# Performance work log

Measured on AMD Instinct MI355X. Metric: run time of the kernel, lower is better.

## Reference

```python
import jax, jax.numpy as jnp
import numpy as np

H, W = 48, 96          # fmap_size
HEADS, DH = 4, 128     # BoTNet attention defaults
EPS = 1e-5


def rel_to_abs(x):
    # x: (B, L, 2L-1) relative logits -> (B, L, L) absolute logits
    b, l, _ = x.shape
    x = jnp.pad(x, ((0, 0), (0, 0), (0, 1)))          # (B, L, 2L)
    x = x.reshape(b, l * 2 * l)
    x = jnp.pad(x, ((0, 0), (0, l - 1)))               # (B, (L+1)(2L-1))
    x = x.reshape(b, l + 1, 2 * l - 1)
    return x[:, :l, l - 1:]


def relative_logits_1d(q, rel_k):
    # q: (b, n, X, Y, d), rel_k: (2Y-1, d) -> (b, n, X, X, Y, Y)
    b, n, X, Y, d = q.shape
    logits = jnp.einsum('bnxyd,rd->bnxyr', q, rel_k)
    logits = rel_to_abs(logits.reshape(b * n * X, Y, 2 * Y - 1)).reshape(b, n, X, Y, Y)
    return jnp.broadcast_to(logits[:, :, :, None], (b, n, X, X, Y, Y))


def rel_pos_bias(q, rel_h, rel_w):
    # q: (b, n, H*W, d) already scaled -> (b, n, H*W, H*W)
    b, n, _, d = q.shape
    q2 = q.reshape(b, n, H, W, d)
    lw = relative_logits_1d(q2, rel_w)                     # (b,n,hq,hk,wq,wk)
    lw = lw.transpose(0, 1, 2, 4, 3, 5).reshape(b, n, H * W, H * W)
    qt = q2.transpose(0, 1, 3, 2, 4)                       # (b,n,W,H,d)
    lh = relative_logits_1d(qt, rel_h)                     # (b,n,wq,wk,hq,hk)
    lh = lh.transpose(0, 1, 4, 2, 5, 3).reshape(b, n, H * W, H * W)
    return lw + lh


def bn(x, g, b_, m, v):
    # inference-mode BatchNorm2d over channel dim of (B,C,H,W)
    inv = g * jax.lax.rsqrt(v + EPS)
    return (x - m[:, None, None]) * inv[:, None, None] + b_[:, None, None]


def reference(x, w_in, bn1_g, bn1_b, bn1_m, bn1_v, w_qkv, rel_h, rel_w,
              w_out, bn2_g, bn2_b, bn2_m, bn2_v, w_head, b_head):
    b = x.shape[0]
    # Self_Attn (BoTNet BottleBlock): 1x1 conv down-proj + BN + ReLU
    h1 = jax.nn.relu(bn(jnp.einsum('bcxy,oc->boxy', x, w_in), bn1_g, bn1_b, bn1_m, bn1_v))
    # qkv via 1x1 conv (no bias), chunk into q,k,v blocks along channels
    qkv = jnp.einsum('bcxy,oc->boxy', h1, w_qkv).reshape(b, 3, HEADS, DH, H * W)
    q = qkv[:, 0].transpose(0, 1, 3, 2) * (DH ** -0.5)     # (b, heads, HW, dh)
    k = qkv[:, 1].transpose(0, 1, 3, 2)
    v = qkv[:, 2].transpose(0, 1, 3, 2)
    sim = jnp.einsum('bhid,bhjd->bhij', q, k) + rel_pos_bias(q, rel_h, rel_w)
    attn = jax.nn.softmax(sim, axis=-1)
    out = jnp.einsum('bhij,bhjd->bhid', attn, v)           # (b, heads, HW, dh)
    out = out.transpose(0, 1, 3, 2).reshape(b, HEADS * DH, H, W)
    # 1x1 conv up-proj + BN, residual (dim==dim_out so shortcut=identity), ReLU
    h2 = bn(jnp.einsum('bcxy,oc->boxy', out, w_out), bn2_g, bn2_b, bn2_m, bn2_v)
    fm = jax.nn.relu(h2 + x)
    # Head's final 1x1 conv projection to out_planes
    return jnp.einsum('bcxy,oc->boxy', fm, w_head) + b_head[None, :, None, None]


def setup_inputs() -> dict:
    key = jax.random.key(0)
    ks = jax.random.split(key, 8)
    f = lambda k, s, sc: jax.random.normal(k, s, jnp.float32) * sc
    C_IN, C_MID, C_ATT, C_OUT = 256, 256, 64, 19
    return {
        'x': jax.random.normal(ks[0], (1, C_IN, H, W), jnp.float32),
        'w_in': f(ks[1], (C_ATT, C_IN), 0.05),
        'bn1_g': jnp.ones(C_ATT, jnp.float32), 'bn1_b': jnp.zeros(C_ATT, jnp.float32),
        'bn1_m': jnp.zeros(C_ATT, jnp.float32), 'bn1_v': jnp.ones(C_ATT, jnp.float32),
        'w_qkv': f(ks[2], (3 * HEADS * DH, C_ATT), 0.05),
        'rel_h': f(ks[3], (2 * H - 1, DH), 0.09),
        'rel_w': f(ks[4], (2 * W - 1, DH), 0.09),
        'w_out': f(ks[5], (C_MID, HEADS * DH), 0.02),
        'bn2_g': jnp.ones(C_MID, jnp.float32), 'bn2_b': jnp.zeros(C_MID, jnp.float32),
        'bn2_m': jnp.zeros(C_MID, jnp.float32), 'bn2_v': jnp.ones(C_MID, jnp.float32),
        'w_head': f(ks[6], (C_OUT, C_MID), 0.05),
        'b_head': jnp.zeros(C_OUT, jnp.float32),
    }
```

## Files before the change

kernel.cpp:

```cpp
#include <hip/hip_runtime.h>


typedef __attribute__((ext_vector_type(4))) float f32x4;
typedef __attribute__((ext_vector_type(8))) short s16x8;
typedef __attribute__((ext_vector_type(4))) unsigned short u16x4;

#define HW_N 4608
#define EPS 1e-5f
#define QSCALE 0.08838834764831845f

__device__ __forceinline__ unsigned short f2bf(float f) {
  unsigned u = __builtin_bit_cast(unsigned, f);
  u += 0x7fffu + ((u >> 16) & 1u);
  return (unsigned short)(u >> 16);
}
__device__ __forceinline__ float bf2f(unsigned short s) {
  return __builtin_bit_cast(float, ((unsigned)s) << 16);
}

__global__ __launch_bounds__(256) void conv1_kernel(
    const float* __restrict__ x, const float* __restrict__ w,
    const float* __restrict__ gg, const float* __restrict__ bb,
    const float* __restrict__ mm, const float* __restrict__ vv,
    float* __restrict__ h1)
{
  __shared__ __align__(16) unsigned char smA[16384];
  __shared__ __align__(16) unsigned char smB[16384];
  const int tid = (int)threadIdx.x;
  const int tx = tid & 15, ty = tid >> 4;
  const int p0 = (int)blockIdx.x * 64;
  float acc[4][4] = {};
  for (int ch = 0; ch < 4; ++ch) {
    __syncthreads();
#pragma unroll
    for (int pass = 0; pass < 4; ++pass) {
      int c4 = tid + pass * 256;
      int oc = c4 >> 4, cc4 = c4 & 15;
      f32x4 a = *(const f32x4*)(w + oc * 256 + ch * 64 + cc4 * 4);
#pragma unroll
      for (int k = 0; k < 4; ++k) {
        int cc = cc4 * 4 + k;
        *(float*)(smA + cc * 256 + ((oc * 4) ^ ((cc & 7) << 4))) = a[k];
      }
      int cc = c4 >> 4, pp4 = c4 & 15;
      f32x4 b = *(const f32x4*)(x + (ch * 64 + cc) * HW_N + p0 + pp4 * 4);
      *(f32x4*)(smB + cc * 256 + ((pp4 * 16) ^ ((cc & 7) << 4))) = b;
    }
    __syncthreads();
#pragma unroll 8
    for (int cc = 0; cc < 64; ++cc) {
      f32x4 av = *(const f32x4*)(smA + cc * 256 + ((ty * 16) ^ ((cc & 7) << 4)));
      f32x4 bv = *(const f32x4*)(smB + cc * 256 + ((tx * 16) ^ ((cc & 7) << 4)));
#pragma unroll
      for (int i = 0; i < 4; ++i)
#pragma unroll
        for (int j = 0; j < 4; ++j) acc[i][j] = fmaf(av[i], bv[j], acc[i][j]);
    }
  }
#pragma unroll
  for (int i = 0; i < 4; ++i) {
    int oc = ty * 4 + i;
    float inv = gg[oc] * rsqrtf(vv[oc] + EPS);
    float bia = bb[oc] - mm[oc] * inv;
    f32x4 o;
#pragma unroll
    for (int j = 0; j < 4; ++j) o[j] = fmaxf(acc[i][j] * inv + bia, 0.f);
    *(f32x4*)(h1 + oc * HW_N + p0 + tx * 4) = o;
  }
}

__global__ __launch_bounds__(256) void convqkv_kernel(
    const float* __restrict__ h1, const float* __restrict__ w,
    unsigned short* __restrict__ qb, unsigned short* __restrict__ kb,
    unsigned short* __restrict__ vb)
{
  __shared__ __align__(16) unsigned char smA[16384];
  __shared__ __align__(16) unsigned char smB[16384];
  const int tid = (int)threadIdx.x;
  const int tx = tid & 15, ty = tid >> 4;
  const int p0 = (int)blockIdx.x * 64;
  const int o0 = (int)blockIdx.y * 64;
  float acc[4][4] = {};
#pragma unroll
  for (int pass = 0; pass < 4; ++pass) {
    int c4 = tid + pass * 256;
    int oc = c4 >> 4, cc4 = c4 & 15;
    f32x4 a = *(const f32x4*)(w + (o0 + oc) * 64 + cc4 * 4);
#pragma unroll
    for (int k = 0; k < 4; ++k) {
      int cc = cc4 * 4 + k;
      *(float*)(smA + cc * 256 + ((oc * 4) ^ ((cc & 7) << 4))) = a[k];
    }
    int cc = c4 >> 4, pp4 = c4 & 15;
    f32x4 b = *(const f32x4*)(h1 + cc * HW_N + p0 + pp4 * 4);
    *(f32x4*)(smB + cc * 256 + ((pp4 * 16) ^ ((cc & 7) << 4))) = b;
  }
  __syncthreads();
#pragma unroll 8
  for (int cc = 0; cc < 64; ++cc) {
    f32x4 av = *(const f32x4*)(smA + cc * 256 + ((tx * 16) ^ ((cc & 7) << 4)));
    f32x4 bv = *(const f32x4*)(smB + cc * 256 + ((ty * 16) ^ ((cc & 7) << 4)));
#pragma unroll
    for (int i = 0; i < 4; ++i)
#pragma unroll
      for (int j = 0; j < 4; ++j) acc[i][j] = fmaf(av[i], bv[j], acc[i][j]);
  }
  const int chunk = o0 >> 9, head = (o0 >> 7) & 3, dbase = o0 & 127;
  if (chunk == 0) {
#pragma unroll
    for (int j = 0; j < 4; ++j) {
      unsigned short pk[4];
#pragma unroll
      for (int i = 0; i < 4; ++i) pk[i] = f2bf(acc[i][j] * QSCALE);
      *(unsigned long long*)(qb + (head * HW_N + p0 + ty * 4 + j) * 128 + dbase + tx * 4) =
          *(unsigned long long*)pk;
    }
  } else if (chunk == 1) {
#pragma unroll
    for (int j = 0; j < 4; ++j) {
      unsigned short pk[4];
#pragma unroll
      for (int i = 0; i < 4; ++i) pk[i] = f2bf(acc[i][j]);
      *(unsigned long long*)(kb + (head * HW_N + p0 + ty * 4 + j) * 128 + dbase + tx * 4) =
          *(unsigned long long*)pk;
    }
  } else {
#pragma unroll
    for (int i = 0; i < 4; ++i) {
      unsigned short pk[4];
#pragma unroll
      for (int j = 0; j < 4; ++j) pk[j] = f2bf(acc[i][j]);
      *(unsigned long long*)(vb + (head * 128 + dbase + tx * 4 + i) * HW_N + p0 + ty * 4) =
          *(unsigned long long*)pk;
    }
  }
}

__global__ __launch_bounds__(256) void relpre_mfma(
    const unsigned short* __restrict__ qb, const float* __restrict__ rel,
    float* __restrict__ outp, int mode)
{
  __shared__ __align__(16) unsigned char sm[36864];
  const int bx = (int)blockIdx.x, h = (int)blockIdx.y;
  const int tid = (int)threadIdx.x;
  const int wv = tid >> 6, g = (tid >> 4) & 3, c = tid & 15;
  const int NA = mode ? 96 : 48;
  const int NB = mode ? 48 : 96;
  const int TC = NB >> 4;
  const int roff = mode ? (47 - bx) : (95 - bx);
  unsigned char* const smQ = sm;
  unsigned char* const smR = sm + NA * 256;

  for (int ch = tid; ch < (NA + NB) * 16; ch += 256) {
    if (ch < NA * 16) {
      int i = ch >> 4, d8 = ch & 15;
      int p = mode ? (bx * 96 + i) : (i * 96 + bx);
      s16x8 v = *(const s16x8*)(qb + ((size_t)h * HW_N + p) * 128 + d8 * 8);
      *(s16x8*)(smQ + i * 256 + ((d8 * 16) ^ ((i & 7) << 4))) = v;
    } else {
      int c2 = ch - NA * 16;
      int j = c2 >> 4, d8 = c2 & 15;
      const float* rp = rel + (roff + j) * 128 + d8 * 8;
      f32x4 r0 = *(const f32x4*)(rp);
      f32x4 r1 = *(const f32x4*)(rp + 4);
      s16x8 pk;
#pragma unroll
      for (int e = 0; e < 4; ++e) {
        pk[e] = (short)f2bf(r0[e]);
        pk[4 + e] = (short)f2bf(r1[e]);
      }
      *(s16x8*)(smR + j * 256 + ((d8 * 16) ^ ((j & 7) << 4))) = pk;
    }
  }
  __syncthreads();

  const int swzc = (c & 7) << 4;
  for (int tile = wv; tile < 18; tile += 4) {
    const int tr = tile / TC, tc = tile % TC;
    f32x4 acc = {};
#pragma unroll
    for (int kk = 0; kk < 4; ++kk) {
      const int koff = (kk * 64 + g * 16) ^ swzc;
      s16x8 a = *(const s16x8*)(smQ + (tr * 16 + c) * 256 + koff);
      s16x8 b = *(const s16x8*)(smR + (tc * 16 + c) * 256 + koff);
      acc = __builtin_amdgcn_mfma_f32_16x16x32_bf16(a, b, acc, 0, 0, 0);
    }
#pragma unroll
    for (int j = 0; j < 4; ++j) {
      int i = tr * 16 + g * 4 + j;
      int n = tc * 16 + c;
      if (mode == 0)
        outp[((size_t)h * HW_N + i * 96 + bx) * 96 + n] = acc[j];
      else
        outp[((size_t)h * HW_N + bx * 96 + i) * 48 + n] = acc[j];
    }
  }
}

__global__ __launch_bounds__(256, 2) void attn_kernel(
    const unsigned short* __restrict__ qb,
    const unsigned short* __restrict__ kbuf,
    const unsigned short* __restrict__ vbuf,
    const float* __restrict__ RW,
    const float* __restrict__ RH,
    unsigned short* __restrict__ Opart,
    float* __restrict__ mlbuf)
{
  __shared__ __align__(16) unsigned char sm[36864];
  unsigned char* const smK = sm;
  unsigned char* const smV = sm + 12288;
  unsigned char* const smP = sm + 28672;

  const int tid = (int)threadIdx.x;
  const int wv = tid >> 6;
  const int g = (tid >> 4) & 3;
  const int c = tid & 15;
  const int swzc = (c & 7) << 4;
  const int pswz_c = ((c >> 2) << 5) | ((c & 1) << 4);

  int lin = (int)blockIdx.x + 72 * ((int)blockIdx.y + 4 * (int)blockIdx.z);
  const int grp = lin & 15, mem = lin >> 4;
  const int h = grp & 3, kh = grp >> 2, qt = mem;

  const int qbase = qt * 64 + wv * 16;
  const int woff = wv * 2048;

  {
    s16x8 z = {};
    *(s16x8*)(smP + tid * 16) = z;
    *(s16x8*)(smP + 4096 + tid * 16) = z;
    int d = tid >> 1, k6 = 6 + (tid & 1);
    *(s16x8*)(smV + d * 128 + ((k6 * 16) ^ ((d & 7) << 4))) = z;
  }

  s16x8 aq[4];
  {
    const unsigned short* qrow = qb + ((size_t)h * HW_N + qbase + c) * 128 + g * 8;
#pragma unroll
    for (int kk = 0; kk < 4; ++kk) aq[kk] = *(const s16x8*)(qrow + kk * 32);
  }

  float bw0[3][4], bw1[3][4];
#pragma unroll
  for (int r = 0; r < 4; ++r) {
    const float* rwrow = RW + ((size_t)h * HW_N + qbase + g * 4 + r) * 96 + c;
#pragma unroll
    for (int kb = 0; kb < 3; ++kb) {
      bw0[kb][r] = rwrow[kb * 16];
      bw1[kb][r] = rwrow[48 + kb * 16];
    }
  }
  float rh_pre[4];
#pragma unroll
  for (int r = 0; r < 4; ++r)
    rh_pre[r] = (c < 12)
        ? RH[((size_t)h * HW_N + qbase + g * 4 + r) * 48 + kh * 12 + c] : 0.f;

  f32x4 o[8];
#pragma unroll
  for (int cb = 0; cb < 8; ++cb) o[cb] = {};
  float mrun[4], lrun[4];
#pragma unroll
  for (int r = 0; r < 4; ++r) { mrun[r] = -1e30f; lrun[r] = 0.f; }

  const unsigned short* kbase = kbuf + ((size_t)h * HW_N + kh * 1152) * 128;
  const unsigned short* vbase = vbuf + (size_t)h * 128 * HW_N + kh * 1152;

  const int kkey = tid >> 4, kd8 = tid & 15;
  const int swzk = (kkey & 7) << 4;
  const int vd0 = tid / 6, vk0 = tid % 6;
  const int vd1 = (tid + 256) / 6, vk1 = (tid + 256) % 6;
  const int vd2 = (tid + 512) / 6, vk2 = (tid + 512) % 6;

  s16x8 sK0, sK1, sK2, sV0, sV1, sV2;
  {
    const unsigned short* kp = kbase + kkey * 128 + kd8 * 8;
    sK0 = *(const s16x8*)(kp);
    sK1 = *(const s16x8*)(kp + 16 * 128);
    sK2 = *(const s16x8*)(kp + 32 * 128);
    sV0 = *(const s16x8*)(vbase + vd0 * HW_N + vk0 * 8);
    sV1 = *(const s16x8*)(vbase + vd1 * HW_N + vk1 * 8);
    sV2 = *(const s16x8*)(vbase + vd2 * HW_N + vk2 * 8);
  }

  for (int t = 0; t < 24; ++t) {
    __syncthreads();
    *(s16x8*)(smK + kkey * 256 + ((kd8 * 16) ^ swzk)) = sK0;
    *(s16x8*)(smK + (kkey + 16) * 256 + ((kd8 * 16) ^ swzk)) = sK1;
    *(s16x8*)(smK + (kkey + 32) * 256 + ((kd8 * 16) ^ swzk)) = sK2;
    *(s16x8*)(smV + vd0 * 128 + ((vk0 * 16) ^ ((vd0 & 7) << 4))) = sV0;
    *(s16x8*)(smV + vd1 * 128 + ((vk1 * 16) ^ ((vd1 & 7) << 4))) = sV1;
    *(s16x8*)(smV + vd2 * 128 + ((vk2 * 16) ^ ((vd2 & 7) << 4))) = sV2;
    if (t < 23) {
      int j0n = (t + 1) * 48;
      const unsigned short* kp = kbase + (j0n + kkey) * 128 + kd8 * 8;
      sK0 = *(const s16x8*)(kp);
      sK1 = *(const s16x8*)(kp + 16 * 128);
      sK2 = *(const s16x8*)(kp + 32 * 128);
      sV0 = *(const s16x8*)(vbase + vd0 * HW_N + j0n + vk0 * 8);
      sV1 = *(const s16x8*)(vbase + vd1 * HW_N + j0n + vk1 * 8);
      sV2 = *(const s16x8*)(vbase + vd2 * HW_N + j0n + vk2 * 8);
    }
    float rh_[4];
    {
      const int hkl = t >> 1;
#pragma unroll
      for (int r = 0; r < 4; ++r) rh_[r] = __shfl(rh_pre[r], hkl, 16);
    }
    __syncthreads();

    f32x4 s0 = {}, s1 = {}, s2 = {};
#pragma unroll
    for (int kk = 0; kk < 4; ++kk) {
      const int inr = kk * 64 + g * 16;
      s16x8 b0 = *(const s16x8*)(smK + c * 256 + (inr ^ swzc));
      s16x8 b1 = *(const s16x8*)(smK + (16 + c) * 256 + (inr ^ swzc));
      s16x8 b2 = *(const s16x8*)(smK + (32 + c) * 256 + (inr ^ swzc));
      s0 = __builtin_amdgcn_mfma_f32_16x16x32_bf16(aq[kk], b0, s0, 0, 0, 0);
      s1 = __builtin_amdgcn_mfma_f32_16x16x32_bf16(aq[kk], b1, s1, 0, 0, 0);
      s2 = __builtin_amdgcn_mfma_f32_16x16x32_bf16(aq[kk], b2, s2, 0, 0, 0);
    }

    const bool par = (t & 1) != 0;
    float x0[4], x1[4], x2[4], tm3[4];
    int need = 0;
#pragma unroll
    for (int r = 0; r < 4; ++r) {
      x0[r] = s0[r] + (par ? bw1[0][r] : bw0[0][r]) + rh_[r];
      x1[r] = s1[r] + (par ? bw1[1][r] : bw0[1][r]) + rh_[r];
      x2[r] = s2[r] + (par ? bw1[2][r] : bw0[2][r]) + rh_[r];
      tm3[r] = fmaxf(fmaxf(x0[r], x1[r]), x2[r]);
      need |= (tm3[r] > mrun[r] + 8.f);
    }
    if (__any(need)) {
#pragma unroll
      for (int r = 0; r < 4; ++r) {
        float tg = tm3[r];
        tg = fmaxf(tg, __shfl_xor(tg, 1, 16));
        tg = fmaxf(tg, __shfl_xor(tg, 2, 16));
        tg = fmaxf(tg, __shfl_xor(tg, 4, 16));
        tg = fmaxf(tg, __shfl_xor(tg, 8, 16));
        float mn = fmaxf(mrun[r], tg);
        float fac = __expf(mrun[r] - mn);
        mrun[r] = mn;
        lrun[r] *= fac;
#pragma unroll
        for (int cb = 0; cb < 8; ++cb) o[cb][r] *= fac;
      }
    }
#pragma unroll
    for (int r = 0; r < 4; ++r) {
      float p0 = __expf(x0[r] - mrun[r]);
      float p1 = __expf(x1[r] - mrun[r]);
      float p2 = __expf(x2[r] - mrun[r]);
      lrun[r] += p0 + p1 + p2;
      const int q_ = g * 4 + r;
      unsigned char* prow = smP + woff + q_ * 128;
      const int swzq = ((q_ >> 2) << 5) | ((q_ & 1) << 4);
      *(unsigned short*)(prow + ((c * 2) ^ swzq)) = f2bf(p0);
      *(unsigned short*)(prow + ((32 + c * 2) ^ swzq)) = f2bf(p1);
      *(unsigned short*)(prow + ((64 + c * 2) ^ swzq)) = f2bf(p2);
    }

    s16x8 pa0 = *(const s16x8*)(smP + woff + c * 128 + ((g * 16) ^ pswz_c));
    s16x8 pa1 = *(const s16x8*)(smP + woff + c * 128 + ((64 + g * 16) ^ pswz_c));
#pragma unroll
    for (int cb = 0; cb < 8; ++cb) {
      const unsigned char* vrow = smV + (cb * 16 + c) * 128;
      s16x8 v0 = *(const s16x8*)(vrow + ((g * 16) ^ swzc));
      s16x8 v1 = *(const s16x8*)(vrow + ((64 + g * 16) ^ swzc));
      o[cb] = __builtin_amdgcn_mfma_f32_16x16x32_bf16(pa0, v0, o[cb], 0, 0, 0);
      o[cb] = __builtin_amdgcn_mfma_f32_16x16x32_bf16(pa1, v1, o[cb], 0, 0, 0);
    }
  }

#pragma unroll
  for (int r = 0; r < 4; ++r) {
    lrun[r] += __shfl_xor(lrun[r], 1, 16);
    lrun[r] += __shfl_xor(lrun[r], 2, 16);
    lrun[r] += __shfl_xor(lrun[r], 4, 16);
    lrun[r] += __shfl_xor(lrun[r], 8, 16);
  }

  const int pb = (kh * 4 + h) * HW_N;
#pragma unroll
  for (int r = 0; r < 4; ++r) {
    const int p = qbase + g * 4 + r;
    unsigned short* orow = Opart + ((size_t)pb + p) * 128 + c;
#pragma unroll
    for (int cb = 0; cb < 8; ++cb) orow[cb * 16] = f2bf(o[cb][r]);
    if (c == 0) {
      mlbuf[((size_t)pb + p) * 2 + 0] = mrun[r];
      mlbuf[((size_t)pb + p) * 2 + 1] = lrun[r];
    }
  }
}

__global__ __launch_bounds__(256) void merge_kernel(
    const unsigned short* __restrict__ Opart, const float* __restrict__ mlbuf,
    float* __restrict__ oatt)
{
  int idx = (int)blockIdx.x * 256 + (int)threadIdx.x;
  int d4 = idx & 31;
  int rest = idx >> 5;
  int p = rest % HW_N;
  int h = rest / HW_N;
  float m[4], l[4];
#pragma unroll
  for (int s = 0; s < 4; ++s) {
    int ip = (s * 4 + h) * HW_N + p;
    m[s] = mlbuf[(size_t)ip * 2];
    l[s] = mlbuf[(size_t)ip * 2 + 1];
  }
  float M = fmaxf(fmaxf(m[0], m[1]), fmaxf(m[2], m[3]));
  float a[4], den = 0.f;
#pragma unroll
  for (int s = 0; s < 4; ++s) { a[s] = __expf(m[s] - M); den += a[s] * l[s]; }
  float rd = 1.f / den;
  f32x4 acc = {};
#pragma unroll
  for (int s = 0; s < 4; ++s) {
    int ip = (s * 4 + h) * HW_N + p;
    u16x4 ov = *(const u16x4*)(Opart + (size_t)ip * 128 + d4 * 4);
#pragma unroll
    for (int j = 0; j < 4; ++j) acc[j] = fmaf(a[s], bf2f(ov[j]), acc[j]);
  }
  f32x4 res;
#pragma unroll
  for (int j = 0; j < 4; ++j) res[j] = acc[j] * rd;
  *(f32x4*)(oatt + (size_t)p * 512 + h * 128 + d4 * 4) = res;
}

__global__ __launch_bounds__(256) void convout_kernel(
    const float* __restrict__ oatt, const float* __restrict__ w,
    const float* __restrict__ gg, const float* __restrict__ bb,
    const float* __restrict__ mm, const float* __restrict__ vv,
    const float* __restrict__ x, float* __restrict__ fm)
{
  __shared__ __align__(16) unsigned char smA[16384];
  __shared__ __align__(16) unsigned char smB[16384];
  const int tid = (int)threadIdx.x;
  const int tx = tid & 15, ty = tid >> 4;
  const int p0 = (int)blockIdx.x * 64;
  const int o0 = (int)blockIdx.y * 64;
  float acc[4][4] = {};
  for (int ch = 0; ch < 8; ++ch) {
    __syncthreads();
#pragma unroll
    for (int pass = 0; pass < 4; ++pass) {
      int c4 = tid + pass * 256;
      int oc = c4 >> 4, cc4 = c4 & 15;
      f32x4 a = *(const f32x4*)(w + (o0 + oc) * 512 + ch * 64 + cc4 * 4);
#pragma unroll
      for (int k = 0; k < 4; ++k) {
        int cc = cc4 * 4 + k;
        *(float*)(smA + cc * 256 + ((oc * 4) ^ ((cc & 7) << 4))) = a[k];
      }
      int pl = c4 >> 4, cc4b = c4 & 15;
      f32x4 b = *(const f32x4*)(oatt + (size_t)(p0 + pl) * 512 + ch * 64 + cc4b * 4);
#pragma unroll
      for (int k = 0; k < 4; ++k) {
        int cc = cc4b * 4 + k;
        *(float*)(smB + cc * 256 + ((pl * 4) ^ ((cc & 7) << 4))) = b[k];
      }
    }
    __syncthreads();
#pragma unroll 8
    for (int cc = 0; cc < 64; ++cc) {
      f32x4 av = *(const f32x4*)(smA + cc * 256 + ((ty * 16) ^ ((cc & 7) << 4)));
      f32x4 bv = *(const f32x4*)(smB + cc * 256 + ((tx * 16) ^ ((cc & 7) << 4)));
#pragma unroll
      for (int i = 0; i < 4; ++i)
#pragma unroll
        for (int j = 0; j < 4; ++j) acc[i][j] = fmaf(av[i], bv[j], acc[i][j]);
    }
  }
#pragma unroll
  for (int i = 0; i < 4; ++i) {
    int oc = o0 + ty * 4 + i;
    float inv = gg[oc] * rsqrtf(vv[oc] + EPS);
    float bia = bb[oc] - mm[oc] * inv;
    f32x4 xr = *(const f32x4*)(x + (size_t)oc * HW_N + p0 + tx * 4);
    f32x4 o;
#pragma unroll
    for (int j = 0; j < 4; ++j) o[j] = fmaxf(acc[i][j] * inv + bia + xr[j], 0.f);
    *(f32x4*)(fm + (size_t)oc * HW_N + p0 + tx * 4) = o;
  }
}

__global__ __launch_bounds__(256) void convhead_kernel(
    const float* __restrict__ fm, const float* __restrict__ w,
    const float* __restrict__ bh, float* __restrict__ outp)
{
  __shared__ __align__(16) unsigned char smA[16384];
  __shared__ __align__(16) unsigned char smB[16384];
  const int tid = (int)threadIdx.x;
  const int tx = tid & 15, ty = tid >> 4;
  const int p0 = (int)blockIdx.x * 64;
  float acc[4][4] = {};
  for (int ch = 0; ch < 4; ++ch) {
    __syncthreads();
#pragma unroll
    for (int pass = 0; pass < 4; ++pass) {
      int c4 = tid + pass * 256;
      int oc = c4 >> 4, cc4 = c4 & 15;
      f32x4 a = {};
      if (oc < 19) a = *(const f32x4*)(w + oc * 256 + ch * 64 + cc4 * 4);
#pragma unroll
      for (int k = 0; k < 4; ++k) {
        int cc = cc4 * 4 + k;
        *(float*)(smA + cc * 256 + ((oc * 4) ^ ((cc & 7) << 4))) = a[k];
      }
      int cc = c4 >> 4, pp4 = c4 & 15;
      f32x4 b = *(const f32x4*)(fm + (ch * 64 + cc) * HW_N + p0 + pp4 * 4);
      *(f32x4*)(smB + cc * 256 + ((pp4 * 16) ^ ((cc & 7) << 4))) = b;
    }
    __syncthreads();
#pragma unroll 8
    for (int cc = 0; cc < 64; ++cc) {
      f32x4 av = *(const f32x4*)(smA + cc * 256 + ((ty * 16) ^ ((cc & 7) << 4)));
      f32x4 bv = *(const f32x4*)(smB + cc * 256 + ((tx * 16) ^ ((cc & 7) << 4)));
#pragma unroll
      for (int i = 0; i < 4; ++i)
#pragma unroll
        for (int j = 0; j < 4; ++j) acc[i][j] = fmaf(av[i], bv[j], acc[i][j]);
    }
  }
#pragma unroll
  for (int i = 0; i < 4; ++i) {
    int oc = ty * 4 + i;
    if (oc < 19) {
      f32x4 o;
#pragma unroll
      for (int j = 0; j < 4; ++j) o[j] = acc[i][j] + bh[oc];
      *(f32x4*)(outp + oc * HW_N + p0 + tx * 4) = o;
    }
  }
}

extern "C" void kernel_launch(void* const* d_in, const int* in_sizes, int n_in,
                              void* d_out, int out_size, void* d_ws, size_t ws_size,
                              hipStream_t stream)
{
  const float* x     = (const float*)d_in[0];
  const float* w_in  = (const float*)d_in[1];
  const float* bn1_g = (const float*)d_in[2];
  const float* bn1_b = (const float*)d_in[3];
  const float* bn1_m = (const float*)d_in[4];
  const float* bn1_v = (const float*)d_in[5];
  const float* w_qkv = (const float*)d_in[6];
  const float* rel_h = (const float*)d_in[7];
  const float* rel_w = (const float*)d_in[8];
  const float* w_out = (const float*)d_in[9];
  const float* bn2_g = (const float*)d_in[10];
  const float* bn2_b = (const float*)d_in[11];
  const float* bn2_m = (const float*)d_in[12];
  const float* bn2_v = (const float*)d_in[13];
  const float* w_hd  = (const float*)d_in[14];
  const float* b_hd  = (const float*)d_in[15];

  char* ws = (char*)d_ws;
  float*          h1    = (float*)(ws + 0);
  float*          mlb   = (float*)(ws + 0);
  unsigned short* qb    = (unsigned short*)(ws + 1179648);
  unsigned short* kb    = (unsigned short*)(ws + 5898240);
  unsigned short* vb    = (unsigned short*)(ws + 10616832);
  float*          RW    = (float*)(ws + 15335424);
  float*          RH    = (float*)(ws + 22413312);
  unsigned short* Opart = (unsigned short*)(ws + 25952256);
  float*          oatt  = (float*)(ws + 45121536);
  float*          fm    = (float*)(ws + 54558720);

  conv1_kernel<<<72, 256, 0, stream>>>(x, w_in, bn1_g, bn1_b, bn1_m, bn1_v, h1);
  convqkv_kernel<<<dim3(72, 24), 256, 0, stream>>>(h1, w_qkv, qb, kb, vb);
  relpre_mfma<<<dim3(96, 4), 256, 0, stream>>>(qb, rel_w, RW, 0);
  relpre_mfma<<<dim3(48, 4), 256, 0, stream>>>(qb, rel_h, RH, 1);
  attn_kernel<<<dim3(72, 4, 4), 256, 0, stream>>>(qb, kb, vb, RW, RH, Opart, mlb);
  merge_kernel<<<2304, 256, 0, stream>>>(Opart, mlb, oatt);
  convout_kernel<<<dim3(72, 4), 256, 0, stream>>>(oatt, w_out, bn2_g, bn2_b, bn2_m,
                                                  bn2_v, x, fm);
  convhead_kernel<<<72, 256, 0, stream>>>(fm, w_hd, b_hd, (float*)d_out);
}
```

Baseline: 307.2 us.

## Double query tile in attention, use async K loads, bf16 MFMA output convs

The attention kernel now handles 32 query rows per wave instead of 16, so each K/V tile in LDS is reused across twice as many queries. K tiles are double-buffered and loaded straight into LDS with global_load_lds, and Opart writes are staged through LDS to make them coalesced. The two relpre launches are merged into one, merge/convout/convhead now pass bf16 intermediates, and the out/head 1x1 convs use bf16 MFMA instead of scalar fp32 FMA. The trade-offs are more registers and LDS (lower occupancy), half as many attention blocks, and some added bf16 rounding error.

```diff
diff --git a/kernel.cpp b/kernel.cpp
--- a/kernel.cpp
+++ b/kernel.cpp
@@ -16,6 +16,9 @@
 }
 __device__ __forceinline__ float bf2f(unsigned short s) {
   return __builtin_bit_cast(float, ((unsigned)s) << 16);
+}
+__device__ __forceinline__ void gload_lds16(const void* g, void* l) {
+  __builtin_amdgcn_global_load_lds(g, l, 16, 0, 0);
 }
 
 __global__ __launch_bounds__(256) void conv1_kernel(
@@ -137,17 +140,23 @@
 }
 
 __global__ __launch_bounds__(256) void relpre_mfma(
-    const unsigned short* __restrict__ qb, const float* __restrict__ rel,
-    float* __restrict__ outp, int mode)
+    const unsigned short* __restrict__ qb,
+    const float* __restrict__ rel_h, const float* __restrict__ rel_w,
+    float* __restrict__ RW, float* __restrict__ RH)
 {
   __shared__ __align__(16) unsigned char sm[36864];
-  const int bx = (int)blockIdx.x, h = (int)blockIdx.y;
+  int bxr = (int)blockIdx.x;
+  const int mode = bxr >= 96;
+  const int bx = mode ? bxr - 96 : bxr;
+  const int h = (int)blockIdx.y;
   const int tid = (int)threadIdx.x;
   const int wv = tid >> 6, g = (tid >> 4) & 3, c = tid & 15;
   const int NA = mode ? 96 : 48;
   const int NB = mode ? 48 : 96;
   const int TC = NB >> 4;
   const int roff = mode ? (47 - bx) : (95 - bx);
+  const float* rel = mode ? rel_h : rel_w;
+  float* outp = mode ? RH : RW;
   unsigned char* const smQ = sm;
   unsigned char* const smR = sm + NA * 256;
 
@@ -206,78 +215,82 @@
     unsigned short* __restrict__ Opart,
     float* __restrict__ mlbuf)
 {
-  __shared__ __align__(16) unsigned char sm[36864];
+  __shared__ __align__(16) unsigned char sm[57344];
   unsigned char* const smK = sm;
-  unsigned char* const smV = sm + 12288;
-  unsigned char* const smP = sm + 28672;
+  unsigned char* const smV = sm + 24576;
+  unsigned char* const smP = sm + 40960;
 
   const int tid = (int)threadIdx.x;
   const int wv = tid >> 6;
   const int g = (tid >> 4) & 3;
   const int c = tid & 15;
   const int swzc = (c & 7) << 4;
-  const int pswz_c = ((c >> 2) << 5) | ((c & 1) << 4);
-
-  int lin = (int)blockIdx.x + 72 * ((int)blockIdx.y + 4 * (int)blockIdx.z);
-  const int grp = lin & 15, mem = lin >> 4;
-  const int h = grp & 3, kh = grp >> 2, qt = mem;
-
-  const int qbase = qt * 64 + wv * 16;
-  const int woff = wv * 2048;
+
+  int lin = (int)blockIdx.x + 36 * ((int)blockIdx.y + 4 * (int)blockIdx.z);
+  const int grp = lin & 15, qt = lin >> 4;
+  const int h = grp & 3, kh = grp >> 2;
+
+  const int qbaseW = qt * 128 + wv * 32;
+  const int pb = (kh * 4 + h) * HW_N;
 
   {
     s16x8 z = {};
-    *(s16x8*)(smP + tid * 16) = z;
-    *(s16x8*)(smP + 4096 + tid * 16) = z;
+#pragma unroll
+    for (int i = 0; i < 4; ++i) *(s16x8*)(smP + i * 4096 + tid * 16) = z;
     int d = tid >> 1, k6 = 6 + (tid & 1);
     *(s16x8*)(smV + d * 128 + ((k6 * 16) ^ ((d & 7) << 4))) = z;
   }
 
-  s16x8 aq[4];
-  {
-    const unsigned short* qrow = qb + ((size_t)h * HW_N + qbase + c) * 128 + g * 8;
-#pragma unroll
-    for (int kk = 0; kk < 4; ++kk) aq[kk] = *(const s16x8*)(qrow + kk * 32);
-  }
-
-  float bw0[3][4], bw1[3][4];
-#pragma unroll
-  for (int r = 0; r < 4; ++r) {
-    const float* rwrow = RW + ((size_t)h * HW_N + qbase + g * 4 + r) * 96 + c;
-#pragma unroll
-    for (int kb = 0; kb < 3; ++kb) {
-      bw0[kb][r] = rwrow[kb * 16];
-      bw1[kb][r] = rwrow[48 + kb * 16];
-    }
-  }
-  float rh_pre[4];
-#pragma unroll
-  for (int r = 0; r < 4; ++r)
-    rh_pre[r] = (c < 12)
-        ? RH[((size_t)h * HW_N + qbase + g * 4 + r) * 48 + kh * 12 + c] : 0.f;
-
-  f32x4 o[8];
-#pragma unroll
-  for (int cb = 0; cb < 8; ++cb) o[cb] = {};
-  float mrun[4], lrun[4];
-#pragma unroll
-  for (int r = 0; r < 4; ++r) { mrun[r] = -1e30f; lrun[r] = 0.f; }
-
-  const unsigned short* kbase = kbuf + ((size_t)h * HW_N + kh * 1152) * 128;
+  s16x8 aq[2][4];
+#pragma unroll
+  for (int u = 0; u < 2; ++u) {
+    const unsigned short* qrow = qb + ((size_t)h * HW_N + qbaseW + u * 16 + c) * 128 + g * 8;
+#pragma unroll
+    for (int kk = 0; kk < 4; ++kk) aq[u][kk] = *(const s16x8*)(qrow + kk * 32);
+  }
+
+  float bw0[3][2][4], bw1[3][2][4];
+  float rh_pre[2][4];
+#pragma unroll
+  for (int u = 0; u < 2; ++u)
+#pragma unroll
+    for (int r = 0; r < 4; ++r) {
+      const int q = qbaseW + u * 16 + g * 4 + r;
+      const float* rwrow = RW + ((size_t)h * HW_N + q) * 96 + c;
+#pragma unroll
+      for (int kb = 0; kb < 3; ++kb) {
+        bw0[kb][u][r] = rwrow[kb * 16];
+        bw1[kb][u][r] = rwrow[48 + kb * 16];
+      }
+      rh_pre[u][r] = (c < 12) ? RH[((size_t)h * HW_N + q) * 48 + kh * 12 + c] : 0.f;
+    }
+
+  f32x4 o[2][8];
+#pragma unroll
+  for (int u = 0; u < 2; ++u)
+#pragma unroll
+    for (int cb = 0; cb < 8; ++cb) o[u][cb] = {};
+  float mrun[2][4], lrun[2][4];
+#pragma unroll
+  for (int u = 0; u < 2; ++u)
+#pragma unroll
+    for (int r = 0; r < 4; ++r) { mrun[u][r] = -1e30f; lrun[u][r] = 0.f; }
+
+  const char* kbase = (const char*)kbuf + ((size_t)h * HW_N + kh * 1152) * 256;
   const unsigned short* vbase = vbuf + (size_t)h * 128 * HW_N + kh * 1152;
 
-  const int kkey = tid >> 4, kd8 = tid & 15;
-  const int swzk = (kkey & 7) << 4;
+  const int krow4 = tid >> 4, kd8 = tid & 15;
+  const int ksrcoff = (kd8 * 16) ^ ((krow4 & 7) << 4);
   const int vd0 = tid / 6, vk0 = tid % 6;
   const int vd1 = (tid + 256) / 6, vk1 = (tid + 256) % 6;
   const int vd2 = (tid + 512) / 6, vk2 = (tid + 512) % 6;
 
-  s16x8 sK0, sK1, sK2, sV0, sV1, sV2;
+  s16x8 sV0, sV1, sV2;
   {
-    const unsigned short* kp = kbase + kkey * 128 + kd8 * 8;
-    sK0 = *(const s16x8*)(kp);
-    sK1 = *(const s16x8*)(kp + 16 * 128);
-    sK2 = *(const s16x8*)(kp + 32 * 128);
+#pragma unroll
+    for (int i = 0; i < 3; ++i)
+      gload_lds16(kbase + (size_t)(i * 16 + krow4) * 256 + ksrcoff,
+                  smK + i * 4096 + wv * 1024);
     sV0 = *(const s16x8*)(vbase + vd0 * HW_N + vk0 * 8);
     sV1 = *(const s16x8*)(vbase + vd1 * HW_N + vk1 * 8);
     sV2 = *(const s16x8*)(vbase + vd2 * HW_N + vk2 * 8);
@@ -285,137 +298,174 @@
 
   for (int t = 0; t < 24; ++t) {
     __syncthreads();
-    *(s16x8*)(smK + kkey * 256 + ((kd8 * 16) ^ swzk)) = sK0;
-    *(s16x8*)(smK + (kkey + 16) * 256 + ((kd8 * 16) ^ swzk)) = sK1;
-    *(s16x8*)(smK + (kkey + 32) * 256 + ((kd8 * 16) ^ swzk)) = sK2;
     *(s16x8*)(smV + vd0 * 128 + ((vk0 * 16) ^ ((vd0 & 7) << 4))) = sV0;
     *(s16x8*)(smV + vd1 * 128 + ((vk1 * 16) ^ ((vd1 & 7) << 4))) = sV1;
     *(s16x8*)(smV + vd2 * 128 + ((vk2 * 16) ^ ((vd2 & 7) << 4))) = sV2;
+    float rh_[2][4];
+#pragma unroll
+    for (int u = 0; u < 2; ++u)
+#pragma unroll
+      for (int r = 0; r < 4; ++r) rh_[u][r] = __shfl(rh_pre[u][r], t >> 1, 16);
+    __syncthreads();
+    const unsigned char* smKb = smK + (t & 1) * 12288;
     if (t < 23) {
-      int j0n = (t + 1) * 48;
-      const unsigned short* kp = kbase + (j0n + kkey) * 128 + kd8 * 8;
-      sK0 = *(const s16x8*)(kp);
-      sK1 = *(const s16x8*)(kp + 16 * 128);
-      sK2 = *(const s16x8*)(kp + 32 * 128);
+      const int nb = (t + 1) & 1;
+#pragma unroll
+      for (int i = 0; i < 3; ++i)
+        gload_lds16(kbase + (size_t)((t + 1) * 48 + i * 16 + krow4) * 256 + ksrcoff,
+                    smK + nb * 12288 + i * 4096 + wv * 1024);
+      const int j0n = (t + 1) * 48;
       sV0 = *(const s16x8*)(vbase + vd0 * HW_N + j0n + vk0 * 8);
       sV1 = *(const s16x8*)(vbase + vd1 * HW_N + j0n + vk1 * 8);
       sV2 = *(const s16x8*)(vbase + vd2 * HW_N + j0n + vk2 * 8);
     }
-    float rh_[4];
-    {
-      const int hkl = t >> 1;
-#pragma unroll
-      for (int r = 0; r < 4; ++r) rh_[r] = __shfl(rh_pre[r], hkl, 16);
-    }
-    __syncthreads();
-
-    f32x4 s0 = {}, s1 = {}, s2 = {};
+
+    f32x4 s[2][3];
+#pragma unroll
+    for (int u = 0; u < 2; ++u)
+#pragma unroll
+      for (int kb = 0; kb < 3; ++kb) s[u][kb] = {};
 #pragma unroll
     for (int kk = 0; kk < 4; ++kk) {
-      const int inr = kk * 64 + g * 16;
-      s16x8 b0 = *(const s16x8*)(smK + c * 256 + (inr ^ swzc));
-      s16x8 b1 = *(const s16x8*)(smK + (16 + c) * 256 + (inr ^ swzc));
-      s16x8 b2 = *(const s16x8*)(smK + (32 + c) * 256 + (inr ^ swzc));
-      s0 = __builtin_amdgcn_mfma_f32_16x16x32_bf16(aq[kk], b0, s0, 0, 0, 0);
-      s1 = __builtin_amdgcn_mfma_f32_16x16x32_bf16(aq[kk], b1, s1, 0, 0, 0);
-      s2 = __builtin_amdgcn_mfma_f32_16x16x32_bf16(aq[kk], b2, s2, 0, 0, 0);
+      const int inr = (kk * 64 + g * 16) ^ swzc;
+      s16x8 b0 = *(const s16x8*)(smKb + c * 256 + inr);
+      s16x8 b1 = *(const s16x8*)(smKb + (16 + c) * 256 + inr);
+      s16x8 b2 = *(const s16x8*)(smKb + (32 + c) * 256 + inr);
+#pragma unroll
+      for (int u = 0; u < 2; ++u) {
+        s[u][0] = __builtin_amdgcn_mfma_f32_16x16x32_bf16(aq[u][kk], b0, s[u][0], 0, 0, 0);
+        s[u][1] = __builtin_amdgcn_mfma_f32_16x16x32_bf16(aq[u][kk], b1, s[u][1], 0, 0, 0);
+        s[u][2] = __builtin_amdgcn_mfma_f32_16x16x32_bf16(aq[u][kk], b2, s[u][2], 0, 0, 0);
+      }
     }
 
     const bool par = (t & 1) != 0;
-    float x0[4], x1[4], x2[4], tm3[4];
+    float tm3[2][4];
     int need = 0;
 #pragma unroll
+    for (int u = 0; u < 2; ++u)
+#pragma unroll
+      for (int r = 0; r < 4; ++r) {
+        float x0 = s[u][0][r] + (par ? bw1[0][u][r] : bw0[0][u][r]) + rh_[u][r];
+        float x1 = s[u][1][r] + (par ? bw1[1][u][r] : bw0[1][u][r]) + rh_[u][r];
+        float x2 = s[u][2][r] + (par ? bw1[2][u][r] : bw0[2][u][r]) + rh_[u][r];
+        s[u][0][r] = x0; s[u][1][r] = x1; s[u][2][r] = x2;
+        tm3[u][r] = fmaxf(fmaxf(x0, x1), x2);
+        need |= (tm3[u][r] > mrun[u][r] + 8.f);
+      }
+    if (__any(need)) {
+#pragma unroll
+      for (int u = 0; u < 2; ++u)
+#pragma unroll
+        for (int r = 0; r < 4; ++r) {
+          float tg = tm3[u][r];
+          tg = fmaxf(tg, __shfl_xor(tg, 1, 16));
+          tg = fmaxf(tg, __shfl_xor(tg, 2, 16));
+          tg = fmaxf(tg, __shfl_xor(tg, 4, 16));
+          tg = fmaxf(tg, __shfl_xor(tg, 8, 16));
+          float mn = fmaxf(mrun[u][r], tg);
+          float fac = __expf(mrun[u][r] - mn);
+          mrun[u][r] = mn;
+          lrun[u][r] *= fac;
+#pragma unroll
+          for (int cb = 0; cb < 8; ++cb) o[u][cb][r] *= fac;
+        }
+    }
+#pragma unroll
+    for (int u = 0; u < 2; ++u)
+#pragma unroll
+      for (int r = 0; r < 4; ++r) {
+        float p0_ = __expf(s[u][0][r] - mrun[u][r]);
+        float p1_ = __expf(s[u][1][r] - mrun[u][r]);
+        float p2_ = __expf(s[u][2][r] - mrun[u][r]);
+        lrun[u][r] += p0_ + p1_ + p2_;
+        const int row = wv * 32 + u * 16 + g * 4 + r;
+        unsigned char* prow = smP + row * 128;
+        const int sw = (row & 7) << 4;
+        *(unsigned short*)(prow + ((c * 2) ^ sw)) = f2bf(p0_);
+        *(unsigned short*)(prow + ((32 + c * 2) ^ sw)) = f2bf(p1_);
+        *(unsigned short*)(prow + ((64 + c * 2) ^ sw)) = f2bf(p2_);
+      }
+
+    s16x8 pa[2][2];
+#pragma unroll
+    for (int u = 0; u < 2; ++u)
+#pragma unroll
+      for (int ks = 0; ks < 2; ++ks)
+        pa[u][ks] = *(const s16x8*)(smP + (wv * 32 + u * 16 + c) * 128 +
+                                    ((ks * 64 + g * 16) ^ swzc));
+#pragma unroll
+    for (int ks = 0; ks < 2; ++ks)
+#pragma unroll
+      for (int cb = 0; cb < 8; ++cb) {
+        s16x8 v = *(const s16x8*)(smV + (cb * 16 + c) * 128 + ((ks * 64 + g * 16) ^ swzc));
+        o[0][cb] = __builtin_amdgcn_mfma_f32_16x16x32_bf16(pa[0][ks], v, o[0][cb], 0, 0, 0);
+        o[1][cb] = __builtin_amdgcn_mfma_f32_16x16x32_bf16(pa[1][ks], v, o[1][cb], 0, 0, 0);
+      }
+  }
+
+#pragma unroll
+  for (int u = 0; u < 2; ++u)
+#pragma unroll
     for (int r = 0; r < 4; ++r) {
-      x0[r] = s0[r] + (par ? bw1[0][r] : bw0[0][r]) + rh_[r];
-      x1[r] = s1[r] + (par ? bw1[1][r] : bw0[1][r]) + rh_[r];
-      x2[r] = s2[r] + (par ? bw1[2][r] : bw0[2][r]) + rh_[r];
-      tm3[r] = fmaxf(fmaxf(x0[r], x1[r]), x2[r]);
-      need |= (tm3[r] > mrun[r] + 8.f);
-    }
-    if (__any(need)) {
+      lrun[u][r] += __shfl_xor(lrun[u][r], 1, 16);
+      lrun[u][r] += __shfl_xor(lrun[u][r], 2, 16);
+      lrun[u][r] += __shfl_xor(lrun[u][r], 4, 16);
+      lrun[u][r] += __shfl_xor(lrun[u][r], 8, 16);
+    }
+
+  const int l = tid & 63;
+#pragma unroll
+  for (int u = 0; u < 2; ++u) {
+#pragma unroll
+    for (int cb = 0; cb < 8; ++cb)
 #pragma unroll
       for (int r = 0; r < 4; ++r) {
-        float tg = tm3[r];
-        tg = fmaxf(tg, __shfl_xor(tg, 1, 16));
-        tg = fmaxf(tg, __shfl_xor(tg, 2, 16));
-        tg = fmaxf(tg, __shfl_xor(tg, 4, 16));
-        tg = fmaxf(tg, __shfl_xor(tg, 8, 16));
-        float mn = fmaxf(mrun[r], tg);
-        float fac = __expf(mrun[r] - mn);
-        mrun[r] = mn;
-        lrun[r] *= fac;
-#pragma unroll
-        for (int cb = 0; cb < 8; ++cb) o[cb][r] *= fac;
-      }
-    }
-#pragma unroll
-    for (int r = 0; r < 4; ++r) {
-      float p0 = __expf(x0[r] - mrun[r]);
-      float p1 = __expf(x1[r] - mrun[r]);
-      float p2 = __expf(x2[r] - mrun[r]);
-      lrun[r] += p0 + p1 + p2;
-      const int q_ = g * 4 + r;
-      unsigned char* prow = smP + woff + q_ * 128;
-      const int swzq = ((q_ >> 2) << 5) | ((q_ & 1) << 4);
-      *(unsigned short*)(prow + ((c * 2) ^ swzq)) = f2bf(p0);
-      *(unsigned short*)(prow + ((32 + c * 2) ^ swzq)) = f2bf(p1);
-      *(unsigned short*)(prow + ((64 + c * 2) ^ swzq)) = f2bf(p2);
-    }
-
-    s16x8 pa0 = *(const s16x8*)(smP + woff + c * 128 + ((g * 16) ^ pswz_c));
-    s16x8 pa1 = *(const s16x8*)(smP + woff + c * 128 + ((64 + g * 16) ^ pswz_c));
-#pragma unroll
-    for (int cb = 0; cb < 8; ++cb) {
-      const unsigned char* vrow = smV + (cb * 16 + c) * 128;
-      s16x8 v0 = *(const s16x8*)(vrow + ((g * 16) ^ swzc));
-      s16x8 v1 = *(const s16x8*)(vrow + ((64 + g * 16) ^ swzc));
-      o[cb] = __builtin_amdgcn_mfma_f32_16x16x32_bf16(pa0, v0, o[cb], 0, 0, 0);
-      o[cb] = __builtin_amdgcn_mfma_f32_16x16x32_bf16(pa1, v1, o[cb], 0, 0, 0);
-    }
-  }
-
-#pragma unroll
-  for (int r = 0; r < 4; ++r) {
-    lrun[r] += __shfl_xor(lrun[r], 1, 16);
-    lrun[r] += __shfl_xor(lrun[r], 2, 16);
-    lrun[r] += __shfl_xor(lrun[r], 4, 16);
-    lrun[r] += __shfl_xor(lrun[r], 8, 16);
-  }
-
-  const int pb = (kh * 4 + h) * HW_N;
-#pragma unroll
-  for (int r = 0; r < 4; ++r) {
-    const int p = qbase + g * 4 + r;
-    unsigned short* orow = Opart + ((size_t)pb + p) * 128 + c;
-#pragma unroll
-    for (int cb = 0; cb < 8; ++cb) orow[cb * 16] = f2bf(o[cb][r]);
-    if (c == 0) {
-      mlbuf[((size_t)pb + p) * 2 + 0] = mrun[r];
-      mlbuf[((size_t)pb + p) * 2 + 1] = lrun[r];
-    }
+        const int row = g * 4 + r;
+        *(unsigned short*)(smP + wv * 4096 + row * 256 +
+                           (((cb * 16 + c) * 2) ^ ((row & 7) << 4))) = f2bf(o[u][cb][r]);
+      }
+#pragma unroll
+    for (int j = 0; j < 4; ++j) {
+      const int row = j * 4 + (l >> 4);
+      const int off = (l & 15) * 16;
+      s16x8 vd = *(const s16x8*)(smP + wv * 4096 + row * 256 + (off ^ ((row & 7) << 4)));
+      const int p = qbaseW + u * 16 + row;
+      *(s16x8*)((char*)Opart + (size_t)(pb + p) * 256 + off) = vd;
+    }
+  }
+  if (c == 0) {
+#pragma unroll
+    for (int u = 0; u < 2; ++u)
+#pragma unroll
+      for (int r = 0; r < 4; ++r) {
+        const int p = qbaseW + u * 16 + g * 4 + r;
+        mlbuf[((size_t)pb + p) * 2 + 0] = mrun[u][r];
+        mlbuf[((size_t)pb + p) * 2 + 1] = lrun[u][r];
+      }
   }
 }
 
 __global__ __launch_bounds__(256) void merge_kernel(
     const unsigned short* __restrict__ Opart, const float* __restrict__ mlbuf,
-    float* __restrict__ oatt)
+    unsigned short* __restrict__ oatt)
 {
   int idx = (int)blockIdx.x * 256 + (int)threadIdx.x;
   int d4 = idx & 31;
   int rest = idx >> 5;
   int p = rest % HW_N;
   int h = rest / HW_N;
-  float m[4], l[4];
+  float m[4], lv[4];
 #pragma unroll
   for (int s = 0; s < 4; ++s) {
     int ip = (s * 4 + h) * HW_N + p;
     m[s] = mlbuf[(size_t)ip * 2];
-    l[s] = mlbuf[(size_t)ip * 2 + 1];
+    lv[s] = mlbuf[(size_t)ip * 2 + 1];
   }
   float M = fmaxf(fmaxf(m[0], m[1]), fmaxf(m[2], m[3]));
   float a[4], den = 0.f;
 #pragma unroll
-  for (int s = 0; s < 4; ++s) { a[s] = __expf(m[s] - M); den += a[s] * l[s]; }
+  for (int s = 0; s < 4; ++s) { a[s] = __expf(m[s] - M); den += a[s] * lv[s]; }
   float rd = 1.f / den;
   f32x4 acc = {};
 #pragma unroll
@@ -425,117 +475,157 @@
 #pragma unroll
     for (int j = 0; j < 4; ++j) acc[j] = fmaf(a[s], bf2f(ov[j]), acc[j]);
   }
-  f32x4 res;
-#pragma unroll
-  for (int j = 0; j < 4; ++j) res[j] = acc[j] * rd;
-  *(f32x4*)(oatt + (size_t)p * 512 + h * 128 + d4 * 4) = res;
+  u16x4 res;
+#pragma unroll
+  for (int j = 0; j < 4; ++j) res[j] = f2bf(acc[j] * rd);
+  *(u16x4*)(oatt + (size_t)p * 512 + h * 128 + d4 * 4) = res;
 }
 
 __global__ __launch_bounds__(256) void convout_kernel(
-    const float* __restrict__ oatt, const float* __restrict__ w,
+    const unsigned short* __restrict__ oatt, const float* __restrict__ w,
     const float* __restrict__ gg, const float* __restrict__ bb,
     const float* __restrict__ mm, const float* __restrict__ vv,
-    const float* __restrict__ x, float* __restrict__ fm)
-{
-  __shared__ __align__(16) unsigned char smA[16384];
+    const float* __restrict__ x, unsigned short* __restrict__ fm)
+{
+  __shared__ __align__(16) unsigned char smA[8192];
   __shared__ __align__(16) unsigned char smB[16384];
   const int tid = (int)threadIdx.x;
-  const int tx = tid & 15, ty = tid >> 4;
-  const int p0 = (int)blockIdx.x * 64;
+  const int wv = tid >> 6, g = (tid >> 4) & 3, c = tid & 15;
+  const int p0 = (int)blockIdx.x * 128;
   const int o0 = (int)blockIdx.y * 64;
-  float acc[4][4] = {};
+  const int swzc = (c & 7) << 4;
+  const int aoc = tid >> 2, aq4 = tid & 3;
+  const int brow = tid >> 3, bcol = (tid & 7) * 16;
+  f32x4 acc[8];
+#pragma unroll
+  for (int cb = 0; cb < 8; ++cb) acc[cb] = {};
+
   for (int ch = 0; ch < 8; ++ch) {
     __syncthreads();
 #pragma unroll
-    for (int pass = 0; pass < 4; ++pass) {
-      int c4 = tid + pass * 256;
-      int oc = c4 >> 4, cc4 = c4 & 15;
-      f32x4 a = *(const f32x4*)(w + (o0 + oc) * 512 + ch * 64 + cc4 * 4);
-#pragma unroll
-      for (int k = 0; k < 4; ++k) {
-        int cc = cc4 * 4 + k;
-        *(float*)(smA + cc * 256 + ((oc * 4) ^ ((cc & 7) << 4))) = a[k];
-      }
-      int pl = c4 >> 4, cc4b = c4 & 15;
-      f32x4 b = *(const f32x4*)(oatt + (size_t)(p0 + pl) * 512 + ch * 64 + cc4b * 4);
-#pragma unroll
-      for (int k = 0; k < 4; ++k) {
-        int cc = cc4b * 4 + k;
-        *(float*)(smB + cc * 256 + ((pl * 4) ^ ((cc & 7) << 4))) = b[k];
-      }
-    }
-    __syncthreads();
-#pragma unroll 8
-    for (int cc = 0; cc < 64; ++cc) {
-      f32x4 av = *(const f32x4*)(smA + cc * 256 + ((ty * 16) ^ ((cc & 7) << 4)));
-      f32x4 bv = *(const f32x4*)(smB + cc * 256 + ((tx * 16) ^ ((cc & 7) << 4)));
-#pragma unroll
-      for (int i = 0; i < 4; ++i)
-#pragma unroll
-        for (int j = 0; j < 4; ++j) acc[i][j] = fmaf(av[i], bv[j], acc[i][j]);
-    }
-  }
+    for (int i = 0; i < 4; ++i)
+      gload_lds16((const char*)oatt + (size_t)(p0 + i * 32 + brow) * 1024 + ch * 128 +
+                      (bcol ^ ((brow & 7) << 4)),
+                  smB + i * 4096 + wv * 1024);
+    {
+      const float* wp = w + (size_t)(o0 + aoc) * 512 + ch * 64 + aq4 * 16;
+      f32x4 a0 = *(const f32x4*)(wp);
+      f32x4 a1 = *(const f32x4*)(wp + 4);
+      f32x4 a2 = *(const f32x4*)(wp + 8);
+      f32x4 a3 = *(const f32x4*)(wp + 12);
+      s16x8 w0, w1;
+#pragma unroll
+      for (int e = 0; e < 4; ++e) {
+        w0[e] = (short)f2bf(a0[e]); w0[4 + e] = (short)f2bf(a1[e]);
+        w1[e] = (short)f2bf(a2[e]); w1[4 + e] = (short)f2bf(a3[e]);
+      }
+      *(s16x8*)(smA + aoc * 128 + ((aq4 * 32) ^ ((aoc & 7) << 4))) = w0;
+      *(s16x8*)(smA + aoc * 128 + ((aq4 * 32 + 16) ^ ((aoc & 7) << 4))) = w1;
+    }
+    __syncthreads();
+#pragma unroll
+    for (int kk = 0; kk < 2; ++kk) {
+      s16x8 a = *(const s16x8*)(smA + (wv * 16 + c) * 128 + ((kk * 64 + g * 16) ^ swzc));
+#pragma unroll
+      for (int cb = 0; cb < 8; ++cb) {
+        s16x8 b = *(const s16x8*)(smB + (cb * 16 + c) * 128 + ((kk * 64 + g * 16) ^ swzc));
+        acc[cb] = __builtin_amdgcn_mfma_f32_16x16x32_bf16(a, b, acc[cb], 0, 0, 0);
+      }
+    }
+  }
+
+  __syncthreads();
+  float inv[4], bia[4];
+#pragma unroll
+  for (int r = 0; r < 4; ++r) {
+    int oc = o0 + wv * 16 + g * 4 + r;
+    inv[r] = gg[oc] * rsqrtf(vv[oc] + EPS);
+    bia[r] = bb[oc] - mm[oc] * inv[r];
+  }
+#pragma unroll
+  for (int cb = 0; cb < 8; ++cb)
+#pragma unroll
+    for (int r = 0; r < 4; ++r) {
+      int oc = o0 + wv * 16 + g * 4 + r;
+      int p = p0 + cb * 16 + c;
+      float v = fmaxf(acc[cb][r] * inv[r] + bia[r] + x[(size_t)oc * HW_N + p], 0.f);
+      *(unsigned short*)(smB + (cb * 16 + c) * 128 +
+                         (((wv * 16 + g * 4 + r) * 2) ^ swzc)) = f2bf(v);
+    }
+  __syncthreads();
 #pragma unroll
   for (int i = 0; i < 4; ++i) {
-    int oc = o0 + ty * 4 + i;
-    float inv = gg[oc] * rsqrtf(vv[oc] + EPS);
-    float bia = bb[oc] - mm[oc] * inv;
-    f32x4 xr = *(const f32x4*)(x + (size_t)oc * HW_N + p0 + tx * 4);
-    f32x4 o;
-#pragma unroll
-    for (int j = 0; j < 4; ++j) o[j] = fmaxf(acc[i][j] * inv + bia + xr[j], 0.f);
-    *(f32x4*)(fm + (size_t)oc * HW_N + p0 + tx * 4) = o;
+    int row = i * 32 + brow;
+    s16x8 vd = *(const s16x8*)(smB + row * 128 + (bcol ^ ((row & 7) << 4)));
+    *(s16x8*)((char*)fm + (size_t)(p0 + row) * 512 + o0 * 2 + bcol) = vd;
   }
 }
 
 __global__ __launch_bounds__(256) void convhead_kernel(
-    const float* __restrict__ fm, const float* __restrict__ w,
+    const unsigned short* __restrict__ fm, const float* __restrict__ w,
     const float* __restrict__ bh, float* __restrict__ outp)
 {
-  __shared__ __align__(16) unsigned char smA[16384];
+  __shared__ __align__(16) unsigned char smA[4096];
   __shared__ __align__(16) unsigned char smB[16384];
   const int tid = (int)threadIdx.x;
-  const int tx = tid & 15, ty = tid >> 4;
-  const int p0 = (int)blockIdx.x * 64;
-  float acc[4][4] = {};
+  const int wv = tid >> 6, g = (tid >> 4) & 3, c = tid & 15;
+  const int p0 = (int)blockIdx.x * 128;
+  const int swzc = (c & 7) << 4;
+  const int aoc = tid >> 3, aq8 = tid & 7;
+  const int brow = tid >> 3, bcol = (tid & 7) * 16;
+  f32x4 acc[2][2];
+#pragma unroll
+  for (int u = 0; u < 2; ++u)
+#pragma unroll
+    for (int cbi = 0; cbi < 2; ++cbi) acc[u][cbi] = {};
+
   for (int ch = 0; ch < 4; ++ch) {
     __syncthreads();
 #pragma unroll
-    for (int pass = 0; pass < 4; ++pass) {
-      int c4 = tid + pass * 256;
-      int oc = c4 >> 4, cc4 = c4 & 15;
-      f32x4 a = {};
-      if (oc < 19) a = *(const f32x4*)(w + oc * 256 + ch * 64 + cc4 * 4);
-#pragma unroll
-      for (int k = 0; k < 4; ++k) {
-        int cc = cc4 * 4 + k;
-        *(float*)(smA + cc * 256 + ((oc * 4) ^ ((cc & 7) << 4))) = a[k];
-      }
-      int cc = c4 >> 4, pp4 = c4 & 15;
-      f32x4 b = *(const f32x4*)(fm + (ch * 64 + cc) * HW_N + p0 + pp4 * 4);
-      *(f32x4*)(smB + cc * 256 + ((pp4 * 16) ^ ((cc & 7) << 4))) = b;
-    }
-    __syncthreads();
-#pragma unroll 8
-    for (int cc = 0; cc < 64; ++cc) {
-      f32x4 av = *(const f32x4*)(smA + cc * 256 + ((ty * 16) ^ ((cc & 7) << 4)));
-      f32x4 bv = *(const f32x4*)(smB + cc * 256 + ((tx * 16) ^ ((cc & 7) << 4)));
-#pragma unroll
-      for (int i = 0; i < 4; ++i)
-#pragma unroll
-        for (int j = 0; j < 4; ++j) acc[i][j] = fmaf(av[i], bv[j], acc[i][j]);
-    }
-  }
-#pragma unroll
-  for (int i = 0; i < 4; ++i) {
-    int oc = ty * 4 + i;
-    if (oc < 19) {
-      f32x4 o;
-#pragma unroll
-      for (int j = 0; j < 4; ++j) o[j] = acc[i][j] + bh[oc];
-      *(f32x4*)(outp + oc * HW_N + p0 + tx * 4) = o;
-    }
-  }
+    for (int i = 0; i < 4; ++i)
+      gload_lds16((const char*)fm + (size_t)(p0 + i * 32 + brow) * 512 + ch * 128 +
+                      (bcol ^ ((brow & 7) << 4)),
+                  smB + i * 4096 + wv * 1024);
+    {
+      s16x8 w0 = {};
+      if (aoc < 19) {
+        const float* wp = w + (size_t)aoc * 256 + ch * 64 + aq8 * 8;
+        f32x4 a0 = *(const f32x4*)(wp);
+        f32x4 a1 = *(const f32x4*)(wp + 4);
+#pragma unroll
+        for (int e = 0; e < 4; ++e) {
+          w0[e] = (short)f2bf(a0[e]);
+          w0[4 + e] = (short)f2bf(a1[e]);
+        }
+      }
+      *(s16x8*)(smA + aoc * 128 + ((aq8 * 16) ^ ((aoc & 7) << 4))) = w0;
+    }
+    __syncthreads();
+#pragma unroll
+    for (int kk = 0; kk < 2; ++kk) {
+      s16x8 a0 = *(const s16x8*)(smA + c * 128 + ((kk * 64 + g * 16) ^ swzc));
+      s16x8 a1 = *(const s16x8*)(smA + (16 + c) * 128 + ((kk * 64 + g * 16) ^ swzc));
+#pragma unroll
+      for (int cbi = 0; cbi < 2; ++cbi) {
+        int cb = wv * 2 + cbi;
+        s16x8 b = *(const s16x8*)(smB + (cb * 16 + c) * 128 + ((kk * 64 + g * 16) ^ swzc));
+        acc[0][cbi] = __builtin_amdgcn_mfma_f32_16x16x32_bf16(a0, b, acc[0][cbi], 0, 0, 0);
+        acc[1][cbi] = __builtin_amdgcn_mfma_f32_16x16x32_bf16(a1, b, acc[1][cbi], 0, 0, 0);
+      }
+    }
+  }
+#pragma unroll
+  for (int u = 0; u < 2; ++u)
+#pragma unroll
+    for (int cbi = 0; cbi < 2; ++cbi)
+#pragma unroll
+      for (int r = 0; r < 4; ++r) {
+        int oc = u * 16 + g * 4 + r;
+        if (oc < 19) {
+          int p = p0 + (wv * 2 + cbi) * 16 + c;
+          outp[(size_t)oc * HW_N + p] = acc[u][cbi][r] + bh[oc];
+        }
+      }
 }
 
 extern "C" void kernel_launch(void* const* d_in, const int* in_sizes, int n_in,
@@ -568,16 +658,15 @@
   float*          RW    = (float*)(ws + 15335424);
   float*          RH    = (float*)(ws + 22413312);
   unsigned short* Opart = (unsigned short*)(ws + 25952256);
-  float*          oatt  = (float*)(ws + 45121536);
-  float*          fm    = (float*)(ws + 54558720);
+  unsigned short* oatt  = (unsigned short*)(ws + 44826624);
+  unsigned short* fm    = (unsigned short*)(ws + 49545216);
 
   conv1_kernel<<<72, 256, 0, stream>>>(x, w_in, bn1_g, bn1_b, bn1_m, bn1_v, h1);
   convqkv_kernel<<<dim3(72, 24), 256, 0, stream>>>(h1, w_qkv, qb, kb, vb);
-  relpre_mfma<<<dim3(96, 4), 256, 0, stream>>>(qb, rel_w, RW, 0);
-  relpre_mfma<<<dim3(48, 4), 256, 0, stream>>>(qb, rel_h, RH, 1);
-  attn_kernel<<<dim3(72, 4, 4), 256, 0, stream>>>(qb, kb, vb, RW, RH, Opart, mlb);
+  relpre_mfma<<<dim3(144, 4), 256, 0, stream>>>(qb, rel_h, rel_w, RW, RH);
+  attn_kernel<<<dim3(36, 4, 4), 256, 0, stream>>>(qb, kb, vb, RW, RH, Opart, mlb);
   merge_kernel<<<2304, 256, 0, stream>>>(Opart, mlb, oatt);
-  convout_kernel<<<dim3(72, 4), 256, 0, stream>>>(oatt, w_out, bn2_g, bn2_b, bn2_m,
+  convout_kernel<<<dim3(36, 4), 256, 0, stream>>>(oatt, w_out, bn2_g, bn2_b, bn2_m,
                                                   bn2_v, x, fm);
-  convhead_kernel<<<72, 256, 0, stream>>>(fm, w_hd, b_hd, (float*)d_out);
-}
+  convhead_kernel<<<36, 256, 0, stream>>>(fm, w_hd, b_hd, (float*)d_out);
+}
```

Result: slower. 359.0 us (+16.9%).
